# Kernel tuning notes

Measured on AMD Instinct MI355X. Metric: run time of the kernel, lower is better.

## Reference

```python
import jax, jax.numpy as jnp
import numpy as np

VOCAB, INPUT, HIDDEN = 100, 512, 1024
BATCH, SEQ = 64, 512


def setup_inputs() -> dict:
    key = jax.random.key(0)
    ks = jax.random.split(key, 12)
    s = 0.02
    inp = {
        "X": jax.random.randint(ks[0], (BATCH, SEQ), 0, VOCAB, dtype=jnp.int64 if jax.config.jax_enable_x64 else jnp.int32),
        "h0": jnp.zeros((BATCH, HIDDEN), jnp.float32),
        "c0": jnp.zeros((BATCH, HIDDEN), jnp.float32),
        "emb": jax.random.normal(ks[1], (VOCAB, INPUT), jnp.float32) * s,
        "Wf_w": jax.random.normal(ks[2], (HIDDEN, INPUT + HIDDEN), jnp.float32) * s,
        "Wf_b": jnp.zeros((HIDDEN,), jnp.float32),
        "Wi_w": jax.random.normal(ks[3], (HIDDEN, INPUT + HIDDEN), jnp.float32) * s,
        "Wi_b": jnp.zeros((HIDDEN,), jnp.float32),
        "Wo_w": jax.random.normal(ks[4], (HIDDEN, INPUT + HIDDEN), jnp.float32) * s,
        "Wo_b": jnp.zeros((HIDDEN,), jnp.float32),
        "Wg_w": jax.random.normal(ks[5], (HIDDEN, INPUT + HIDDEN), jnp.float32) * s,
        "Wg_b": jnp.zeros((HIDDEN,), jnp.float32),
    }
    return inp


def reference(X, h0, c0, emb, Wf_w, Wf_b, Wi_w, Wi_b, Wo_w, Wo_b, Wg_w, Wg_b):
    # Fuse the 4 gate Linears into one GEMM (same math, concatenated rows).
    W = jnp.concatenate([Wf_w, Wi_w, Wo_w, Wg_w], axis=0)   # [4H, I+H]
    b = jnp.concatenate([Wf_b, Wi_b, Wo_b, Wg_b], axis=0)   # [4H]
    H = Wf_w.shape[0]

    xs = emb[X]                       # [B, S, I]
    xs = jnp.swapaxes(xs, 0, 1)       # [S, B, I] for scan over time

    def step(carry, x_t):
        h, c = carry
        combined = jnp.concatenate([x_t, h], axis=1)          # [B, I+H]
        z = combined @ W.T + b                                # [B, 4H]
        ft = jax.nn.sigmoid(z[:, 0*H:1*H])
        it = jax.nn.sigmoid(z[:, 1*H:2*H])
        ot = jax.nn.sigmoid(z[:, 2*H:3*H])
        gt = jnp.tanh(z[:, 3*H:4*H])
        c_t = ft * c + it * gt
        h_t = ot * jnp.tanh(c_t)
        return (h_t, c_t), h_t

    (h_f, c_f), hs = jax.lax.scan(step, (h0, c0), xs)
    latent = jnp.swapaxes(hs, 0, 1)   # [B, S, H]
    return latent, (h_f, c_f)
```

## Files before the change

kernel.cpp:

```cpp
#include <hip/hip_runtime.h>


typedef _Float16 f16x8 __attribute__((ext_vector_type(8)));
typedef float    f32x4 __attribute__((ext_vector_type(4)));
typedef unsigned int u32x4 __attribute__((ext_vector_type(4)));

#define VOCABN 100

__global__ void k0_zxtable(const float* __restrict__ emb,
                           const float* __restrict__ Wf, const float* __restrict__ bf,
                           const float* __restrict__ Wi, const float* __restrict__ bi,
                           const float* __restrict__ Wo, const float* __restrict__ bo,
                           const float* __restrict__ Wg, const float* __restrict__ bg_,
                           float* __restrict__ zx) {
  const int bid = blockIdx.x;
  const int g = bid >> 6, chunk = bid & 63;
  const float* W = (g==0)?Wf:(g==1)?Wi:(g==2)?Wo:Wg;
  const float* B = (g==0)?bf:(g==1)?bi:(g==2)?bo:bg_;
  __shared__ float Wl[16][516];
  const int tid = threadIdx.x;
  for (int i = tid; i < 2048; i += 256) {
    int r = i >> 7, c4 = i & 127;
    float4 v = *(const float4*)&W[(size_t)(chunk*16 + r)*1536 + c4*4];
    Wl[r][c4*4+0]=v.x; Wl[r][c4*4+1]=v.y; Wl[r][c4*4+2]=v.z; Wl[r][c4*4+3]=v.w;
  }
  __syncthreads();
  const int u = tid & 15, vi = tid >> 4;
  for (int v0 = 0; v0 < VOCABN; v0 += 16) {
    int v = v0 + vi;
    if (v < VOCABN) {
      const float* er = emb + (size_t)v*512;
      float acc = 0.f;
      #pragma unroll 8
      for (int k = 0; k < 512; k++) acc += er[k]*Wl[u][k];
      zx[(size_t)v*4096 + g*1024 + chunk*16 + u] = acc + B[chunk*16 + u];
    }
  }
}

__global__ void k1_prep(const float* __restrict__ Wf, const float* __restrict__ Wi,
                        const float* __restrict__ Wo, const float* __restrict__ Wg,
                        _Float16* __restrict__ Whh) {
  const int bid = blockIdx.x, tid = threadIdx.x;
  #pragma unroll
  for (int i = 0; i < 4; i++) {
    int F = bid*1024 + i*256 + tid;
    int g = F >> 18;
    int rem = F & ((1<<18)-1);
    int n = rem >> 8, k4 = rem & 255;
    const float* W = (g==0)?Wf:(g==1)?Wi:(g==2)?Wo:Wg;
    float4 v = *(const float4*)&W[(size_t)n*1536 + 512 + k4*4];
    _Float16 h4[4] = {(_Float16)v.x,(_Float16)v.y,(_Float16)v.z,(_Float16)v.w};
    *(unsigned long long*)&Whh[((size_t)g<<20) + (n<<10) + (k4<<2)] =
        *(unsigned long long*)h4;
  }
}

__global__ __launch_bounds__(512, 2) void lstm_main(
    const int* __restrict__ X, const float* __restrict__ h0,
    const float* __restrict__ c0, const float* __restrict__ zx,
    const _Float16* __restrict__ Whh, _Float16* __restrict__ hx,
    int* __restrict__ flags, float* out)
{
  const int bid = blockIdx.x;
  const int bg  = bid >> 5;
  const int js  = bid & 31;
  const int tid = threadIdx.x;
  const int w   = tid >> 6;
  const int lane = tid & 63;
  const int lm = lane & 15, lh = lane >> 4;

  __shared__ alignas(16) _Float16 hs[16*1024];
  __shared__ float zsh[8][132];

  f16x8 bw[32];
  {
    const _Float16* wp = Whh + ((size_t)(w>>1)<<20)
                       + ((size_t)(js*32 + (w&1)*16 + lm)<<10) + (lh<<3);
    #pragma unroll
    for (int kk = 0; kk < 32; kk++) {
      asm volatile("global_load_dwordx4 %0, %1, off"
                   : "=&v"(bw[kk]) : "v"(wp + kk*32));
    }
    asm volatile("s_waitcnt vmcnt(0)");
    __builtin_amdgcn_sched_barrier(0);
  }

  const int sr = tid >> 6, sc = tid & 63;
  const int fidx = (bg << 5) + (sc >> 1);

  const int b = (tid >> 5) & 7, u = tid & 31;
  const int brow = bg*8 + b, ucol = js*32 + u;
  float c = 0.f;
  const int* Xr = nullptr;
  if (tid < 256) {
    c = c0[(size_t)brow*1024 + ucol];
    Xr = X + (size_t)brow*512;
  }
  float* latp = out + (size_t)brow*512*1024 + ucol;

  char* hrow_w = (char*)hs + (sr << 11);
  const char* hrow_r = (const char*)hs + (lm << 11);
  const int sww = (sr & 7) << 4, swr = (lm & 7) << 4;

  for (int t = 0; t < 512; t++) {
    float zx0=0.f, zx1=0.f, zx2=0.f, zx3=0.f;
    if (tid < 256) {
      int xv = Xr[t];
      const float* p = zx + (size_t)xv*4096 + ucol;
      zx0 = p[0]; zx1 = p[1024]; zx2 = p[2048]; zx3 = p[3072];
    }

    if (t == 0) {
      const float* s0 = h0 + ((size_t)(bg*8+sr)<<10) + (sc<<4);
      float4 f0 = *(const float4*)(s0+0),  f1 = *(const float4*)(s0+4);
      float4 f2 = *(const float4*)(s0+8),  f3 = *(const float4*)(s0+12);
      _Float16 hh[16] = {(_Float16)f0.x,(_Float16)f0.y,(_Float16)f0.z,(_Float16)f0.w,
                         (_Float16)f1.x,(_Float16)f1.y,(_Float16)f1.z,(_Float16)f1.w,
                         (_Float16)f2.x,(_Float16)f2.y,(_Float16)f2.z,(_Float16)f2.w,
                         (_Float16)f3.x,(_Float16)f3.y,(_Float16)f3.z,(_Float16)f3.w};
      int off = (sc << 5) ^ sww;
      *(u32x4*)(hrow_w + off)        = *(u32x4*)&hh[0];
      *(u32x4*)(hrow_w + (off ^ 16)) = *(u32x4*)&hh[8];
    } else {
      while (__hip_atomic_load(&flags[fidx], __ATOMIC_RELAXED,
                               __HIP_MEMORY_SCOPE_AGENT) < t) {}
      const _Float16* src = hx + (((t-1)&1)<<16) + ((size_t)(bg*8+sr)<<10) + (sc<<4);
      u32x4 va, vb;
      asm volatile(
        "global_load_dwordx4 %0, %2, off sc1\n\t"
        "global_load_dwordx4 %1, %2, off offset:16 sc1\n\t"
        "s_waitcnt vmcnt(0)"
        : "=&v"(va), "=&v"(vb) : "v"(src));
      int off = (sc << 5) ^ sww;
      *(u32x4*)(hrow_w + off)        = va;
      *(u32x4*)(hrow_w + (off ^ 16)) = vb;
    }
    __syncthreads();

    f32x4 a0={0,0,0,0}, a1={0,0,0,0}, a2={0,0,0,0}, a3={0,0,0,0};
    #pragma unroll
    for (int kk = 0; kk < 32; kk += 4) {
      f16x8 x0 = *(const f16x8*)(hrow_r + ((((kk+0)<<6) + (lh<<4)) ^ swr));
      f16x8 x1 = *(const f16x8*)(hrow_r + ((((kk+1)<<6) + (lh<<4)) ^ swr));
      f16x8 x2 = *(const f16x8*)(hrow_r + ((((kk+2)<<6) + (lh<<4)) ^ swr));
      f16x8 x3 = *(const f16x8*)(hrow_r + ((((kk+3)<<6) + (lh<<4)) ^ swr));
      a0 = __builtin_amdgcn_mfma_f32_16x16x32_f16(x0, bw[kk+0], a0, 0, 0, 0);
      a1 = __builtin_amdgcn_mfma_f32_16x16x32_f16(x1, bw[kk+1], a1, 0, 0, 0);
      a2 = __builtin_amdgcn_mfma_f32_16x16x32_f16(x2, bw[kk+2], a2, 0, 0, 0);
      a3 = __builtin_amdgcn_mfma_f32_16x16x32_f16(x3, bw[kk+3], a3, 0, 0, 0);
    }
    f32x4 z4 = (a0 + a1) + (a2 + a3);
    if (lh < 2) {
      #pragma unroll
      for (int r4 = 0; r4 < 4; r4++) zsh[lh*4 + r4][w*16 + lm] = z4[r4];
    }
    __syncthreads();

    float h = 0.f;
    if (tid < 256) {
      float zf = zsh[b][u]      + zx0;
      float zi = zsh[b][32+u]   + zx1;
      float zo = zsh[b][64+u]   + zx2;
      float zg = zsh[b][96+u]   + zx3;
      float fg = 1.f/(1.f + __expf(-zf));
      float ig = 1.f/(1.f + __expf(-zi));
      float og = 1.f/(1.f + __expf(-zo));
      float e2g = __expf(2.f*zg);
      float gg = 1.f - 2.f/(e2g + 1.f);
      c = fg*c + ig*gg;
      float e2c = __expf(2.f*c);
      h = og*(1.f - 2.f/(e2c + 1.f));
      if (t < 511) {
        _Float16 hf = (_Float16)h;
        unsigned short hu = __builtin_bit_cast(unsigned short, hf);
        unsigned pu = (unsigned)__shfl_xor((int)hu, 1);
        if ((u & 1) == 0) {
          unsigned word = (unsigned)hu | (pu << 16);
          __hip_atomic_store((unsigned*)(hx + ((t&1)<<16) + ((size_t)brow<<10) + ucol),
                             word, __ATOMIC_RELAXED, __HIP_MEMORY_SCOPE_AGENT);
        }
      }
    }
    __syncthreads();
    if (tid == 0 && t < 511)
      __hip_atomic_store(&flags[bid], t+1, __ATOMIC_RELAXED, __HIP_MEMORY_SCOPE_AGENT);
    if (tid < 256) {
      __builtin_nontemporal_store(h, latp + (size_t)t*1024);
      if (t == 511) {
        out[33554432 + ((size_t)brow<<10) + ucol] = h;
        out[33619968 + ((size_t)brow<<10) + ucol] = c;
      }
    }
  }
}

extern "C" void kernel_launch(void* const* d_in, const int* in_sizes, int n_in,
                              void* d_out, int out_size, void* d_ws, size_t ws_size,
                              hipStream_t stream) {
  const int*   X   = (const int*)  d_in[0];
  const float* h0  = (const float*)d_in[1];
  const float* c0  = (const float*)d_in[2];
  const float* emb = (const float*)d_in[3];
  const float* Wf  = (const float*)d_in[4];  const float* bf = (const float*)d_in[5];
  const float* Wi  = (const float*)d_in[6];  const float* bi = (const float*)d_in[7];
  const float* Wo  = (const float*)d_in[8];  const float* bo = (const float*)d_in[9];
  const float* Wg  = (const float*)d_in[10]; const float* bg = (const float*)d_in[11];
  float* out = (float*)d_out;

  char* ws = (char*)d_ws;
  float*    zx    = (float*)   ws;
  _Float16* Whh   = (_Float16*)(ws + 1638400);
  _Float16* hx    = (_Float16*)(ws + 1638400 + 8388608);
  int*      flags = (int*)     (ws + 1638400 + 8388608 + 262144);

  hipMemsetAsync(flags, 0, 256*sizeof(int), stream);
  k0_zxtable<<<256, 256, 0, stream>>>(emb, Wf, bf, Wi, bi, Wo, bo, Wg, bg, zx);
  k1_prep<<<1024, 256, 0, stream>>>(Wf, Wi, Wo, Wg, Whh);
  lstm_main<<<256, 512, 0, stream>>>(X, h0, c0, zx, Whh, hx, flags, out);
}
```

Measured before the change: 1.580 ms.

## Replace per-step flag handshake with sentinel-polled 4-slot hidden-state ring buffer

Removes the separate per-block flag array and the extra barrier before publishing the flag. Consumers now spin directly on the hidden-state data until no sentinel words remain, using a 4-deep ring that one block per batch group re-poisons two steps behind. The change also prefetches the next step's input-projection values one iteration ahead, and moves the h0 conversion into the prep kernel. It risks a false match if a real fp16 pair equals the sentinel pattern, and correctness depends on the relaxed-ordering assumptions about when re-poisoning happens.

```diff
diff --git a/kernel.cpp b/kernel.cpp
--- a/kernel.cpp
+++ b/kernel.cpp
@@ -6,6 +6,7 @@
 typedef unsigned int u32x4 __attribute__((ext_vector_type(4)));
 
 #define VOCABN 100
+#define SENTW 0xFEFEFEFEu
 
 __global__ void k0_zxtable(const float* __restrict__ emb,
                            const float* __restrict__ Wf, const float* __restrict__ bf,
@@ -40,37 +41,45 @@
 
 __global__ void k1_prep(const float* __restrict__ Wf, const float* __restrict__ Wi,
                         const float* __restrict__ Wo, const float* __restrict__ Wg,
-                        _Float16* __restrict__ Whh) {
+                        const float* __restrict__ h0,
+                        _Float16* __restrict__ Whh, _Float16* __restrict__ hxbuf) {
   const int bid = blockIdx.x, tid = threadIdx.x;
-  #pragma unroll
-  for (int i = 0; i < 4; i++) {
-    int F = bid*1024 + i*256 + tid;
-    int g = F >> 18;
-    int rem = F & ((1<<18)-1);
-    int n = rem >> 8, k4 = rem & 255;
-    const float* W = (g==0)?Wf:(g==1)?Wi:(g==2)?Wo:Wg;
-    float4 v = *(const float4*)&W[(size_t)n*1536 + 512 + k4*4];
+  if (bid < 1024) {
+    #pragma unroll
+    for (int i = 0; i < 4; i++) {
+      int F = bid*1024 + i*256 + tid;
+      int g = F >> 18;
+      int rem = F & ((1<<18)-1);
+      int n = rem >> 8, k4 = rem & 255;
+      const float* W = (g==0)?Wf:(g==1)?Wi:(g==2)?Wo:Wg;
+      float4 v = *(const float4*)&W[(size_t)n*1536 + 512 + k4*4];
+      _Float16 h4[4] = {(_Float16)v.x,(_Float16)v.y,(_Float16)v.z,(_Float16)v.w};
+      *(unsigned long long*)&Whh[((size_t)g<<20) + (n<<10) + (k4<<2)] =
+          *(unsigned long long*)h4;
+    }
+  } else {
+    int j = bid - 1024;
+    int base = j*1024 + tid*4;
+    float4 v = *(const float4*)&h0[base];
     _Float16 h4[4] = {(_Float16)v.x,(_Float16)v.y,(_Float16)v.z,(_Float16)v.w};
-    *(unsigned long long*)&Whh[((size_t)g<<20) + (n<<10) + (k4<<2)] =
-        *(unsigned long long*)h4;
+    *(unsigned long long*)&hxbuf[3*65536 + base] = *(unsigned long long*)h4;
   }
 }
 
 __global__ __launch_bounds__(512, 2) void lstm_main(
-    const int* __restrict__ X, const float* __restrict__ h0,
-    const float* __restrict__ c0, const float* __restrict__ zx,
-    const _Float16* __restrict__ Whh, _Float16* __restrict__ hx,
-    int* __restrict__ flags, float* out)
+    const int* __restrict__ X, const float* __restrict__ c0,
+    const float* __restrict__ zx, const _Float16* __restrict__ Whh,
+    _Float16* __restrict__ hxbuf, float* out)
 {
   const int bid = blockIdx.x;
   const int bg  = bid >> 5;
   const int js  = bid & 31;
   const int tid = threadIdx.x;
   const int w   = tid >> 6;
-  const int lane = tid & 63;
-  const int lm = lane & 15, lh = lane >> 4;
-
-  __shared__ alignas(16) _Float16 hs[16*1024];
+  const int l   = tid & 63;
+  const int lm = l & 15, lh = l >> 4;
+
+  __shared__ alignas(16) _Float16 hs[16384];
   __shared__ float zsh[8][132];
 
   f16x8 bw[32];
@@ -86,8 +95,10 @@
     __builtin_amdgcn_sched_barrier(0);
   }
 
-  const int sr = tid >> 6, sc = tid & 63;
-  const int fidx = (bg << 5) + (sc >> 1);
+  const int srow = bg*8 + (l & 7);
+  const int soff = (w << 6) + ((l >> 4) << 4);
+  char* lw = (char*)hs + (w << 10) + (l << 4);
+  const char* hb = (const char*)hs + (l << 4);
 
   const int b = (tid >> 5) & 7, u = tid & 31;
   const int brow = bg*8 + b, ucol = js*32 + u;
@@ -99,52 +110,60 @@
   }
   float* latp = out + (size_t)brow*512*1024 + ucol;
 
-  char* hrow_w = (char*)hs + (sr << 11);
-  const char* hrow_r = (const char*)hs + (lm << 11);
-  const int sww = (sr & 7) << 4, swr = (lm & 7) << 4;
+  float zc0=0.f, zc1=0.f, zc2=0.f, zc3=0.f;
+  if (tid < 256) {
+    int xv = Xr[0];
+    const float* p = zx + (size_t)xv*4096 + ucol;
+    zc0 = p[0]; zc1 = p[1024]; zc2 = p[2048]; zc3 = p[3072];
+  }
 
   for (int t = 0; t < 512; t++) {
-    float zx0=0.f, zx1=0.f, zx2=0.f, zx3=0.f;
-    if (tid < 256) {
-      int xv = Xr[t];
+    float zn0=0.f, zn1=0.f, zn2=0.f, zn3=0.f;
+    if (tid < 256 && t < 511) {
+      int xv = Xr[t+1];
       const float* p = zx + (size_t)xv*4096 + ucol;
-      zx0 = p[0]; zx1 = p[1024]; zx2 = p[2048]; zx3 = p[3072];
-    }
-
-    if (t == 0) {
-      const float* s0 = h0 + ((size_t)(bg*8+sr)<<10) + (sc<<4);
-      float4 f0 = *(const float4*)(s0+0),  f1 = *(const float4*)(s0+4);
-      float4 f2 = *(const float4*)(s0+8),  f3 = *(const float4*)(s0+12);
-      _Float16 hh[16] = {(_Float16)f0.x,(_Float16)f0.y,(_Float16)f0.z,(_Float16)f0.w,
-                         (_Float16)f1.x,(_Float16)f1.y,(_Float16)f1.z,(_Float16)f1.w,
-                         (_Float16)f2.x,(_Float16)f2.y,(_Float16)f2.z,(_Float16)f2.w,
-                         (_Float16)f3.x,(_Float16)f3.y,(_Float16)f3.z,(_Float16)f3.w};
-      int off = (sc << 5) ^ sww;
-      *(u32x4*)(hrow_w + off)        = *(u32x4*)&hh[0];
-      *(u32x4*)(hrow_w + (off ^ 16)) = *(u32x4*)&hh[8];
-    } else {
-      while (__hip_atomic_load(&flags[fidx], __ATOMIC_RELAXED,
-                               __HIP_MEMORY_SCOPE_AGENT) < t) {}
-      const _Float16* src = hx + (((t-1)&1)<<16) + ((size_t)(bg*8+sr)<<10) + (sc<<4);
-      u32x4 va, vb;
-      asm volatile(
-        "global_load_dwordx4 %0, %2, off sc1\n\t"
-        "global_load_dwordx4 %1, %2, off offset:16 sc1\n\t"
-        "s_waitcnt vmcnt(0)"
-        : "=&v"(va), "=&v"(vb) : "v"(src));
-      int off = (sc << 5) ^ sww;
-      *(u32x4*)(hrow_w + off)        = va;
-      *(u32x4*)(hrow_w + (off ^ 16)) = vb;
+      zn0 = p[0]; zn1 = p[1024]; zn2 = p[2048]; zn3 = p[3072];
+    }
+
+    {
+      const char* sb = (const char*)hxbuf + (((t-1)&3) << 17) + srow*2048 + soff;
+      u32x4 v0, v1, v2, v3;
+      for (;;) {
+        asm volatile(
+          "global_load_dwordx4 %0, %4, off sc1\n\t"
+          "global_load_dwordx4 %1, %4, off offset:512 sc1\n\t"
+          "global_load_dwordx4 %2, %4, off offset:1024 sc1\n\t"
+          "global_load_dwordx4 %3, %4, off offset:1536 sc1\n\t"
+          "s_waitcnt vmcnt(0)"
+          : "=&v"(v0), "=&v"(v1), "=&v"(v2), "=&v"(v3)
+          : "v"(sb));
+        bool bad = (v0.x==SENTW)|(v0.y==SENTW)|(v0.z==SENTW)|(v0.w==SENTW)
+                 | (v1.x==SENTW)|(v1.y==SENTW)|(v1.z==SENTW)|(v1.w==SENTW)
+                 | (v2.x==SENTW)|(v2.y==SENTW)|(v2.z==SENTW)|(v2.w==SENTW)
+                 | (v3.x==SENTW)|(v3.y==SENTW)|(v3.z==SENTW)|(v3.w==SENTW);
+        if (!bad) break;
+      }
+      *(u32x4*)(lw)         = v0;
+      *(u32x4*)(lw +  8192) = v1;
+      *(u32x4*)(lw + 16384) = v2;
+      *(u32x4*)(lw + 24576) = v3;
     }
     __syncthreads();
+
+    if (js == 0 && t >= 1 && t < 509) {
+      unsigned* rp = (unsigned*)((char*)hxbuf + (((t-2)&3) << 17) + bg*16384) + tid*8;
+      #pragma unroll
+      for (int i = 0; i < 8; i++)
+        __hip_atomic_store(rp + i, SENTW, __ATOMIC_RELAXED, __HIP_MEMORY_SCOPE_AGENT);
+    }
 
     f32x4 a0={0,0,0,0}, a1={0,0,0,0}, a2={0,0,0,0}, a3={0,0,0,0};
     #pragma unroll
     for (int kk = 0; kk < 32; kk += 4) {
-      f16x8 x0 = *(const f16x8*)(hrow_r + ((((kk+0)<<6) + (lh<<4)) ^ swr));
-      f16x8 x1 = *(const f16x8*)(hrow_r + ((((kk+1)<<6) + (lh<<4)) ^ swr));
-      f16x8 x2 = *(const f16x8*)(hrow_r + ((((kk+2)<<6) + (lh<<4)) ^ swr));
-      f16x8 x3 = *(const f16x8*)(hrow_r + ((((kk+3)<<6) + (lh<<4)) ^ swr));
+      f16x8 x0 = *(const f16x8*)(hb + (kk+0)*1024);
+      f16x8 x1 = *(const f16x8*)(hb + (kk+1)*1024);
+      f16x8 x2 = *(const f16x8*)(hb + (kk+2)*1024);
+      f16x8 x3 = *(const f16x8*)(hb + (kk+3)*1024);
       a0 = __builtin_amdgcn_mfma_f32_16x16x32_f16(x0, bw[kk+0], a0, 0, 0, 0);
       a1 = __builtin_amdgcn_mfma_f32_16x16x32_f16(x1, bw[kk+1], a1, 0, 0, 0);
       a2 = __builtin_amdgcn_mfma_f32_16x16x32_f16(x2, bw[kk+2], a2, 0, 0, 0);
@@ -153,16 +172,16 @@
     f32x4 z4 = (a0 + a1) + (a2 + a3);
     if (lh < 2) {
       #pragma unroll
-      for (int r4 = 0; r4 < 4; r4++) zsh[lh*4 + r4][w*16 + lm] = z4[r4];
+      for (int r4 = 0; r4 < 4; r4++)
+        zsh[lh*4 + r4][(w>>1)*32 + (w&1)*16 + lm] = z4[r4];
     }
     __syncthreads();
 
-    float h = 0.f;
     if (tid < 256) {
-      float zf = zsh[b][u]      + zx0;
-      float zi = zsh[b][32+u]   + zx1;
-      float zo = zsh[b][64+u]   + zx2;
-      float zg = zsh[b][96+u]   + zx3;
+      float zf = zsh[b][u]      + zc0;
+      float zi = zsh[b][32+u]   + zc1;
+      float zo = zsh[b][64+u]   + zc2;
+      float zg = zsh[b][96+u]   + zc3;
       float fg = 1.f/(1.f + __expf(-zf));
       float ig = 1.f/(1.f + __expf(-zi));
       float og = 1.f/(1.f + __expf(-zo));
@@ -170,28 +189,26 @@
       float gg = 1.f - 2.f/(e2g + 1.f);
       c = fg*c + ig*gg;
       float e2c = __expf(2.f*c);
-      h = og*(1.f - 2.f/(e2c + 1.f));
+      float h = og*(1.f - 2.f/(e2c + 1.f));
+
       if (t < 511) {
         _Float16 hf = (_Float16)h;
         unsigned short hu = __builtin_bit_cast(unsigned short, hf);
         unsigned pu = (unsigned)__shfl_xor((int)hu, 1);
         if ((u & 1) == 0) {
           unsigned word = (unsigned)hu | (pu << 16);
-          __hip_atomic_store((unsigned*)(hx + ((t&1)<<16) + ((size_t)brow<<10) + ucol),
-                             word, __ATOMIC_RELAXED, __HIP_MEMORY_SCOPE_AGENT);
+          __hip_atomic_store(
+              (unsigned*)((char*)hxbuf + ((t&3) << 17) + brow*2048 + ucol*2),
+              word, __ATOMIC_RELAXED, __HIP_MEMORY_SCOPE_AGENT);
         }
       }
-    }
-    __syncthreads();
-    if (tid == 0 && t < 511)
-      __hip_atomic_store(&flags[bid], t+1, __ATOMIC_RELAXED, __HIP_MEMORY_SCOPE_AGENT);
-    if (tid < 256) {
       __builtin_nontemporal_store(h, latp + (size_t)t*1024);
       if (t == 511) {
         out[33554432 + ((size_t)brow<<10) + ucol] = h;
         out[33619968 + ((size_t)brow<<10) + ucol] = c;
       }
     }
+    zc0 = zn0; zc1 = zn1; zc2 = zn2; zc3 = zn3;
   }
 }
 
@@ -211,11 +228,10 @@
   char* ws = (char*)d_ws;
   float*    zx    = (float*)   ws;
   _Float16* Whh   = (_Float16*)(ws + 1638400);
-  _Float16* hx    = (_Float16*)(ws + 1638400 + 8388608);
-  int*      flags = (int*)     (ws + 1638400 + 8388608 + 262144);
-
-  hipMemsetAsync(flags, 0, 256*sizeof(int), stream);
+  _Float16* hxbuf = (_Float16*)(ws + 1638400 + 8388608);
+
+  hipMemsetAsync(hxbuf, 0xFE, 4*131072, stream);
   k0_zxtable<<<256, 256, 0, stream>>>(emb, Wf, bf, Wi, bi, Wo, bo, Wg, bg, zx);
-  k1_prep<<<1024, 256, 0, stream>>>(Wf, Wi, Wo, Wg, Whh);
-  lstm_main<<<256, 512, 0, stream>>>(X, h0, c0, zx, Whh, hx, flags, out);
-}
+  k1_prep<<<1088, 256, 0, stream>>>(Wf, Wi, Wo, Wg, h0, Whh, hxbuf);
+  lstm_main<<<256, 512, 0, stream>>>(X, c0, zx, Whh, hxbuf, out);
+}
```

Measured after the change: 2.320 ms. 46.9% more time.
